# Performance work log

Measured on AMD Instinct MI355X. Metric: run time of the kernel, lower is better.

The kernel has to match this reference:

```python
import jax, jax.numpy as jnp
import numpy as np

NT, NC, NM = 500_000, 100_000, 20_000   # transaction / client / merchant node counts
E = 500_000                              # edges per relation
IN, EMB, HID, OUT = 128, 64, 64, 2


def _lin_init(k, fan_in, fan_out):
    s = 1.0 / np.sqrt(fan_in)
    k1, k2 = jax.random.split(k)
    W = jax.random.uniform(k1, (fan_in, fan_out), jnp.float32, -s, s)
    b = jax.random.uniform(k2, (fan_out,), jnp.float32, -s, s)
    return W, b


def setup_inputs() -> dict:
    key = jax.random.key(0)
    ks = jax.random.split(key, 24)
    it = iter(range(24))
    d = {}
    d["features"] = jax.random.normal(ks[next(it)], (NT, IN), jnp.float32)
    d["emb_client"] = jax.random.normal(ks[next(it)], (NC, EMB), jnp.float32)
    d["emb_merchant"] = jax.random.normal(ks[next(it)], (NM, EMB), jnp.float32)
    for name, n_src, n_dst in [("c2t", NC, NT), ("m2t", NM, NT), ("t2c", NT, NC), ("t2m", NT, NM)]:
        d[f"src_{name}"] = jax.random.randint(ks[next(it)], (E,), 0, n_src)
        d[f"dst_{name}"] = jax.random.randint(ks[next(it)], (E,), 0, n_dst)
    # per-etype input size: in_size if src==transaction else embedding_size
    in0 = {"c2t": EMB, "m2t": EMB, "t2c": IN, "t2m": IN}
    for e in ["c2t", "m2t", "t2c", "t2m"]:
        d[f"W0_{e}"], d[f"b0_{e}"] = _lin_init(ks[next(it)], in0[e], HID)
        d[f"W1_{e}"], d[f"b1_{e}"] = _lin_init(ks[next(it)], HID, HID)
    d["Wf"], d["bf"] = _lin_init(ks[next(it)], HID, OUT)
    return d


def _seg_mean(msg, dst, n):
    # copy_u 'm' + mean reduce; zero in-degree dst nodes get 0 (DGL semantics)
    s = jax.ops.segment_sum(msg, dst, num_segments=n)
    cnt = jax.ops.segment_sum(jnp.ones((msg.shape[0], 1), msg.dtype), dst, num_segments=n)
    return s / jnp.maximum(cnt, 1.0)


def reference(features, emb_client, emb_merchant,
              src_c2t, dst_c2t, src_m2t, dst_m2t,
              src_t2c, dst_t2c, src_t2m, dst_t2m,
              W0_c2t, b0_c2t, W1_c2t, b1_c2t,
              W0_m2t, b0_m2t, W1_m2t, b1_m2t,
              W0_t2c, b0_t2c, W1_t2c, b1_t2c,
              W0_t2m, b0_t2m, W1_t2m, b1_t2m,
              Wf, bf):
    sizes = {"t": NT, "c": NC, "m": NM}
    edges = {"c2t": ("c", "t", src_c2t, dst_c2t),
             "m2t": ("m", "t", src_m2t, dst_m2t),
             "t2c": ("t", "c", src_t2c, dst_t2c),
             "t2m": ("t", "m", src_t2m, dst_t2m)}

    def rgcn_layer(h, W, b):
        acc = {}
        for e, (s, t, src, dst) in edges.items():
            wh = h[s] @ W[e] + b[e]                 # per-relation Linear on src nodes
            m = _seg_mean(wh[src], dst, sizes[t])   # gather + segment-mean
            acc[t] = acc.get(t, 0.0) + m            # cross-relation 'sum'
        return acc

    W0 = {"c2t": W0_c2t, "m2t": W0_m2t, "t2c": W0_t2c, "t2m": W0_t2m}
    b0 = {"c2t": b0_c2t, "m2t": b0_m2t, "t2c": b0_t2c, "t2m": b0_t2m}
    W1 = {"c2t": W1_c2t, "m2t": W1_m2t, "t2c": W1_t2c, "t2m": W1_t2m}
    b1 = {"c2t": b1_c2t, "m2t": b1_m2t, "t2c": b1_t2c, "t2m": b1_t2m}

    h = {"t": features, "c": emb_client, "m": emb_merchant}
    h = rgcn_layer(h, W0, b0)
    h = {k: jax.nn.leaky_relu(v) for k, v in h.items()}  # applied before layer i!=0
    h = rgcn_layer(h, W1, b1)
    return h["t"] @ Wf + bf                          # final Linear on target ntype
```

## Files before the change

kernel.cpp:

```cpp
#include <hip/hip_runtime.h>
#include <stdint.h>

#define NT 500000
#define NC 100000
#define NM 20000
#define NE 500000

__global__ __launch_bounds__(256) void weq_kernel(const float* __restrict__ W1c,
                                                  const float* __restrict__ b1c,
                                                  const float* __restrict__ W1m,
                                                  const float* __restrict__ b1m,
                                                  const float* __restrict__ Wf,
                                                  float* __restrict__ WeqC,
                                                  float* __restrict__ WeqM,
                                                  float* __restrict__ beq) {
    int t = threadIdx.x;
    if (t < 128) {
        int k = t >> 1, o = t & 1;
        float s = 0.0f;
        for (int j = 0; j < 64; j++) s += W1c[k * 64 + j] * Wf[j * 2 + o];
        WeqC[k * 2 + o] = s;
    } else {
        int k = (t - 128) >> 1, o = t & 1;
        float s = 0.0f;
        for (int j = 0; j < 64; j++) s += W1m[k * 64 + j] * Wf[j * 2 + o];
        WeqM[k * 2 + o] = s;
    }
    if (t < 4) {
        const float* b = (t < 2) ? b1c : b1m;
        int o = t & 1;
        float s = 0.0f;
        for (int j = 0; j < 64; j++) s += b[j] * Wf[j * 2 + o];
        beq[t] = s;
    }
}

__global__ __launch_bounds__(256) void hist4(const int* __restrict__ dTC,
                                             const int* __restrict__ dTM,
                                             const int* __restrict__ dCT,
                                             const int* __restrict__ dMT,
                                             int* __restrict__ cC,
                                             int* __restrict__ cM,
                                             int* __restrict__ cTC,
                                             int* __restrict__ cTM) {
    int id = blockIdx.x * 256 + threadIdx.x;
    int r = id / NE;
    int e = id - r * NE;
    if (r == 0)      atomicAdd(&cC[dTC[e]], 1);
    else if (r == 1) atomicAdd(&cM[dTM[e]], 1);
    else if (r == 2) atomicAdd(&cTC[dCT[e]], 1);
    else if (r == 3) atomicAdd(&cTM[dMT[e]], 1);
}

__global__ __launch_bounds__(256) void blocksum4(const int* __restrict__ cC,
                                                 const int* __restrict__ cM,
                                                 const int* __restrict__ cTC,
                                                 const int* __restrict__ cTM,
                                                 int* __restrict__ blkC,
                                                 int* __restrict__ blkM,
                                                 int* __restrict__ blkTC,
                                                 int* __restrict__ blkTM) {
    int b = blockIdx.x;
    const int* counts; int* blk; int n, bb;
    if (b < 98)       { counts = cC;  blk = blkC;  n = NC; bb = b; }
    else if (b < 118) { counts = cM;  blk = blkM;  n = NM; bb = b - 98; }
    else if (b < 607) { counts = cTC; blk = blkTC; n = NT; bb = b - 118; }
    else              { counts = cTM; blk = blkTM; n = NT; bb = b - 607; }
    int tid = threadIdx.x;
    int base = bb * 1024 + tid * 4;
    int s = 0;
#pragma unroll
    for (int j = 0; j < 4; j++) { int i = base + j; if (i < n) s += counts[i]; }
    for (int off = 32; off; off >>= 1) s += __shfl_down(s, off, 64);
    __shared__ int wsum[4];
    if ((tid & 63) == 0) wsum[tid >> 6] = s;
    __syncthreads();
    if (tid == 0) blk[bb] = wsum[0] + wsum[1] + wsum[2] + wsum[3];
}

__global__ __launch_bounds__(256) void scanblk4(int* __restrict__ blkC,
                                                int* __restrict__ blkM,
                                                int* __restrict__ blkTC,
                                                int* __restrict__ blkTM) {
    int* blk; int nb;
    if (blockIdx.x == 0)      { blk = blkC;  nb = 98; }
    else if (blockIdx.x == 1) { blk = blkM;  nb = 20; }
    else if (blockIdx.x == 2) { blk = blkTC; nb = 489; }
    else                      { blk = blkTM; nb = 489; }
    __shared__ int ps[256];
    int tid = threadIdx.x;
    int i0 = 2 * tid, i1 = i0 + 1;
    int a = (i0 < nb) ? blk[i0] : 0;
    int b = (i1 < nb) ? blk[i1] : 0;
    ps[tid] = a + b;
    __syncthreads();
    for (int off = 1; off < 256; off <<= 1) {
        int t = (tid >= off) ? ps[tid - off] : 0;
        __syncthreads();
        ps[tid] += t;
        __syncthreads();
    }
    int excl = ps[tid] - (a + b);
    if (i0 < nb) blk[i0] = excl;
    if (i1 < nb) blk[i1] = excl + a;
}

__global__ __launch_bounds__(256) void scanfinal4(int* __restrict__ rowPtrC,
                                                  int* __restrict__ cursorC,
                                                  const int* __restrict__ blkC,
                                                  int* __restrict__ rowPtrM,
                                                  int* __restrict__ cursorM,
                                                  const int* __restrict__ blkM,
                                                  int* __restrict__ rowPtrTC,
                                                  int* __restrict__ cursorTC,
                                                  const int* __restrict__ blkTC,
                                                  int* __restrict__ rowPtrTM,
                                                  int* __restrict__ cursorTM,
                                                  const int* __restrict__ blkTM) {
    int b = blockIdx.x;
    int* rowPtr; int* cursor; const int* blkOff; int n, bb;
    if (b < 98)       { rowPtr = rowPtrC;  cursor = cursorC;  blkOff = blkC;  n = NC; bb = b; }
    else if (b < 118) { rowPtr = rowPtrM;  cursor = cursorM;  blkOff = blkM;  n = NM; bb = b - 98; }
    else if (b < 607) { rowPtr = rowPtrTC; cursor = cursorTC; blkOff = blkTC; n = NT; bb = b - 118; }
    else              { rowPtr = rowPtrTM; cursor = cursorTM; blkOff = blkTM; n = NT; bb = b - 607; }
    int tid = threadIdx.x, lane = tid & 63, wv = tid >> 6;
    int base = bb * 1024 + tid * 4;
    int c[4];
#pragma unroll
    for (int j = 0; j < 4; j++) { int i = base + j; c[j] = (i < n) ? rowPtr[i] : 0; }
    int t = c[0] + c[1] + c[2] + c[3];
    int incl = t;
    for (int off = 1; off < 64; off <<= 1) {
        int u = __shfl_up(incl, off, 64);
        if (lane >= off) incl += u;
    }
    int lexcl = incl - t;
    __shared__ int wsum[4], woff[4];
    if (lane == 63) wsum[wv] = incl;
    __syncthreads();
    if (tid == 0) { int a = 0; for (int w = 0; w < 4; w++) { woff[w] = a; a += wsum[w]; } }
    __syncthreads();
    int e = blkOff[bb] + woff[wv] + lexcl;
#pragma unroll
    for (int j = 0; j < 4; j++) {
        int i = base + j;
        if (i < n) {
            rowPtr[i] = e;
            cursor[i] = e;
            if (i == n - 1) rowPtr[n] = e + c[j];
        }
        e += c[j];
    }
}

__global__ __launch_bounds__(256) void scatter4(const int* __restrict__ sTC,
                                                const int* __restrict__ dTC,
                                                int* __restrict__ curC,
                                                int* __restrict__ eidxC,
                                                const int* __restrict__ sTM,
                                                const int* __restrict__ dTM,
                                                int* __restrict__ curM,
                                                int* __restrict__ eidxM,
                                                const int* __restrict__ sCT,
                                                const int* __restrict__ dCT,
                                                int* __restrict__ curTC,
                                                int* __restrict__ eidxTC,
                                                const int* __restrict__ sMT,
                                                const int* __restrict__ dMT,
                                                int* __restrict__ curTM,
                                                int* __restrict__ eidxTM) {
    int id = blockIdx.x * 256 + threadIdx.x;
    int r = id / NE;
    int e = id - r * NE;
    if (r == 0)      { int p = atomicAdd(&curC[dTC[e]], 1);  eidxC[p]  = sTC[e]; }
    else if (r == 1) { int p = atomicAdd(&curM[dTM[e]], 1);  eidxM[p]  = sTM[e]; }
    else if (r == 2) { int p = atomicAdd(&curTC[dCT[e]], 1); eidxTC[p] = sCT[e]; }
    else if (r == 3) { int p = atomicAdd(&curTM[dMT[e]], 1); eidxTM[p] = sMT[e]; }
}

__global__ __launch_bounds__(256) void agg_csr(const float* __restrict__ feat,
                                               const int* __restrict__ rowPtr,
                                               const int* __restrict__ eidx,
                                               float* __restrict__ sum,
                                               int base, int nNodes) {
    int gw = (blockIdx.x * 256 + threadIdx.x) >> 6;
    if (gw >= nNodes) return;
    int lane = threadIdx.x & 63;
    int half = lane >> 5;
    int c4 = (lane & 31) * 4;
    int d = base + gw;
    int s0 = rowPtr[d], s1 = rowPtr[d + 1];
    float a0 = 0.f, a1 = 0.f, a2 = 0.f, a3 = 0.f;
    int i = s0;
    for (; i + 1 < s1; i += 2) {
        int s = eidx[i + half];
        const float4 v = *(const float4*)(feat + (size_t)s * 128 + c4);
        a0 += v.x; a1 += v.y; a2 += v.z; a3 += v.w;
    }
    if (i < s1 && half == 0) {
        int s = eidx[i];
        const float4 v = *(const float4*)(feat + (size_t)s * 128 + c4);
        a0 += v.x; a1 += v.y; a2 += v.z; a3 += v.w;
    }
    a0 += __shfl_xor(a0, 32, 64);
    a1 += __shfl_xor(a1, 32, 64);
    a2 += __shfl_xor(a2, 32, 64);
    a3 += __shfl_xor(a3, 32, 64);
    if (half == 0) {
        float4 o; o.x = a0; o.y = a1; o.z = a2; o.w = a3;
        *(float4*)(sum + (size_t)gw * 128 + c4) = o;
    }
}

__global__ __launch_bounds__(256) void h1proj(const float* __restrict__ sum,
                                              const int* __restrict__ rowPtrB,
                                              const float* __restrict__ W0,
                                              const float* __restrict__ b0,
                                              const float* __restrict__ Weq,
                                              float* __restrict__ p, int n) {
    __shared__ float Ws[128 * 64];
    __shared__ float sums[32 * 128];
    int tid = threadIdx.x;
    int base = blockIdx.x * 32;
    {
        const float4* W4 = (const float4*)W0;
        float4* Ws4 = (float4*)Ws;
        for (int i = tid; i < 128 * 64 / 4; i += 256) Ws4[i] = W4[i];
    }
    {
        const float4* S4 = (const float4*)sum;
        float4* s4 = (float4*)sums;
        for (int i = tid; i < 32 * 128 / 4; i += 256) {
            int r = i >> 5;
            int row = base + r;
            float4 v;
            if (row < n) v = S4[(size_t)base * 32 + i];
            else { v.x = v.y = v.z = v.w = 0.0f; }
            s4[i] = v;
        }
    }
    __syncthreads();
    int col = tid & 63, wv = tid >> 6;
    float acc[8];
#pragma unroll
    for (int r = 0; r < 8; r++) acc[r] = 0.0f;
    const float* srow = &sums[wv * 8 * 128];
    for (int k = 0; k < 128; k += 4) {
        float w0_ = Ws[(k + 0) * 64 + col];
        float w1_ = Ws[(k + 1) * 64 + col];
        float w2_ = Ws[(k + 2) * 64 + col];
        float w3_ = Ws[(k + 3) * 64 + col];
#pragma unroll
        for (int r = 0; r < 8; r++) {
            const float4 s = *(const float4*)&srow[r * 128 + k];
            acc[r] += s.x * w0_ + s.y * w1_ + s.z * w2_ + s.w * w3_;
        }
    }
    float b0c = b0[col];
    float wq0 = Weq[col * 2 + 0], wq1 = Weq[col * 2 + 1];
#pragma unroll
    for (int r = 0; r < 8; r++) {
        int row = base + wv * 8 + r;
        int cn = 0;
        if (row < n) cn = rowPtrB[row + 1] - rowPtrB[row];
        float h = 0.0f;
        if (cn > 0) {
            float v = acc[r] / (float)cn + b0c;
            h = v > 0.0f ? v : 0.01f * v;
        }
        float p0 = h * wq0, p1 = h * wq1;
#pragma unroll
        for (int off = 32; off; off >>= 1) {
            p0 += __shfl_down(p0, off, 64);
            p1 += __shfl_down(p1, off, 64);
        }
        if (col == 0 && row < n) {
            p[(size_t)row * 2 + 0] = p0;
            p[(size_t)row * 2 + 1] = p1;
        }
    }
}

__global__ __launch_bounds__(256) void gather_final(const float* __restrict__ pC,
                                                    const int* __restrict__ rowPtrTC,
                                                    const int* __restrict__ eidxTC,
                                                    const float* __restrict__ pM,
                                                    const int* __restrict__ rowPtrTM,
                                                    const int* __restrict__ eidxTM,
                                                    const float* __restrict__ beq,
                                                    const float* __restrict__ bfv,
                                                    float* __restrict__ out) {
    int i = blockIdx.x * 256 + threadIdx.x;
    if (i >= NT) return;
    float r0 = bfv[0], r1 = bfv[1];
    {
        int s0 = rowPtrTC[i], s1 = rowPtrTC[i + 1];
        if (s1 > s0) {
            float a0 = 0.f, a1 = 0.f;
            for (int e = s0; e < s1; e++) {
                int s = eidxTC[e];
                const float2 v = *(const float2*)(pC + (size_t)s * 2);
                a0 += v.x; a1 += v.y;
            }
            float inv = 1.0f / (float)(s1 - s0);
            r0 += a0 * inv + beq[0];
            r1 += a1 * inv + beq[1];
        }
    }
    {
        int s0 = rowPtrTM[i], s1 = rowPtrTM[i + 1];
        if (s1 > s0) {
            float a0 = 0.f, a1 = 0.f;
            for (int e = s0; e < s1; e++) {
                int s = eidxTM[e];
                const float2 v = *(const float2*)(pM + (size_t)s * 2);
                a0 += v.x; a1 += v.y;
            }
            float inv = 1.0f / (float)(s1 - s0);
            r0 += a0 * inv + beq[2];
            r1 += a1 * inv + beq[3];
        }
    }
    float2 o; o.x = r0; o.y = r1;
    *(float2*)(out + (size_t)i * 2) = o;
}

extern "C" void kernel_launch(void* const* d_in, const int* in_sizes, int n_in,
                              void* d_out, int out_size, void* d_ws, size_t ws_size,
                              hipStream_t stream) {
    const float* feat = (const float*)d_in[0];
    const int* src_c2t = (const int*)d_in[3];
    const int* dst_c2t = (const int*)d_in[4];
    const int* src_m2t = (const int*)d_in[5];
    const int* dst_m2t = (const int*)d_in[6];
    const int* src_t2c = (const int*)d_in[7];
    const int* dst_t2c = (const int*)d_in[8];
    const int* src_t2m = (const int*)d_in[9];
    const int* dst_t2m = (const int*)d_in[10];
    const float* W1_c2t = (const float*)d_in[13];
    const float* b1_c2t = (const float*)d_in[14];
    const float* W1_m2t = (const float*)d_in[17];
    const float* b1_m2t = (const float*)d_in[18];
    const float* W0_t2c = (const float*)d_in[19];
    const float* b0_t2c = (const float*)d_in[20];
    const float* W0_t2m = (const float*)d_in[23];
    const float* b0_t2m = (const float*)d_in[24];
    const float* Wf  = (const float*)d_in[27];
    const float* bfv = (const float*)d_in[28];

    char* ws = (char*)d_ws;
    float* SUM      = (float*)(ws + 0);
    int*   rowPtrC  = (int*)(ws + 25600000);
    int*   rowPtrM  = (int*)(ws + 26000016);
    int*   rowPtrTC = (int*)(ws + 26080032);
    int*   rowPtrTM = (int*)(ws + 28080036);
    int*   cursorC  = (int*)(ws + 30080040);
    int*   cursorM  = (int*)(ws + 30480040);
    int*   cursorTC = (int*)(ws + 30560040);
    int*   cursorTM = (int*)(ws + 32560040);
    int*   eidxC    = (int*)(ws + 34560040);
    int*   eidxM    = (int*)(ws + 36560040);
    int*   eidxTC   = (int*)(ws + 38560040);
    int*   eidxTM   = (int*)(ws + 40560040);
    float* pC       = (float*)(ws + 42560040);
    float* pM       = (float*)(ws + 43360040);
    float* WeqC     = (float*)(ws + 43520040);
    float* WeqM     = (float*)(ws + 43520552);
    float* beq      = (float*)(ws + 43521064);
    int*   blkC     = (int*)(ws + 43521080);
    int*   blkM     = (int*)(ws + 43521472);
    int*   blkTC    = (int*)(ws + 43521552);
    int*   blkTM    = (int*)(ws + 43523508);

    hipMemsetAsync(rowPtrC, 0, 4480040, stream);

    weq_kernel<<<1, 256, 0, stream>>>(W1_c2t, b1_c2t, W1_m2t, b1_m2t, Wf, WeqC, WeqM, beq);

    hist4<<<7813, 256, 0, stream>>>(dst_t2c, dst_t2m, dst_c2t, dst_m2t,
                                    rowPtrC, rowPtrM, rowPtrTC, rowPtrTM);
    blocksum4<<<1096, 256, 0, stream>>>(rowPtrC, rowPtrM, rowPtrTC, rowPtrTM,
                                        blkC, blkM, blkTC, blkTM);
    scanblk4<<<4, 256, 0, stream>>>(blkC, blkM, blkTC, blkTM);
    scanfinal4<<<1096, 256, 0, stream>>>(rowPtrC, cursorC, blkC,
                                         rowPtrM, cursorM, blkM,
                                         rowPtrTC, cursorTC, blkTC,
                                         rowPtrTM, cursorTM, blkTM);
    scatter4<<<7813, 256, 0, stream>>>(src_t2c, dst_t2c, cursorC, eidxC,
                                       src_t2m, dst_t2m, cursorM, eidxM,
                                       src_c2t, dst_c2t, cursorTC, eidxTC,
                                       src_m2t, dst_m2t, cursorTM, eidxTM);

    agg_csr<<<12500, 256, 0, stream>>>(feat, rowPtrC, eidxC, SUM, 0, 50000);
    h1proj<<<1563, 256, 0, stream>>>(SUM, rowPtrC, W0_t2c, b0_t2c, WeqC, pC, 50000);
    agg_csr<<<12500, 256, 0, stream>>>(feat, rowPtrC, eidxC, SUM, 50000, 50000);
    h1proj<<<1563, 256, 0, stream>>>(SUM, rowPtrC + 50000, W0_t2c, b0_t2c, WeqC, pC + 100000, 50000);
    agg_csr<<<5000, 256, 0, stream>>>(feat, rowPtrM, eidxM, SUM, 0, 20000);
    h1proj<<<625, 256, 0, stream>>>(SUM, rowPtrM, W0_t2m, b0_t2m, WeqM, pM, 20000);

    gather_final<<<1954, 256, 0, stream>>>(pC, rowPtrTC, eidxTC,
                                           pM, rowPtrTM, eidxTM,
                                           beq, bfv, (float*)d_out);
}
```

Baseline: 825.7 us.

## Replace CSR build with atomicExch linked-list edge chains per destination

Drops the histogram, block-sum, scan and scatter kernels that built a CSR for each relation. A single kernel now pushes every edge onto a per-destination linked list with atomicExch and stores (src, next) records. Aggregation and the final gather walk these chains and count the degree as they go. This saves four launches and their passes over the count arrays, but it makes each edge visit a dependent pointer chase with poor locality, and aggregation now uses float2 per lane with one edge at a time instead of two edges per wave.

```diff
diff --git a/kernel.cpp b/kernel.cpp
--- a/kernel.cpp
+++ b/kernel.cpp
@@ -35,185 +35,64 @@
     }
 }
 
-__global__ __launch_bounds__(256) void hist4(const int* __restrict__ dTC,
-                                             const int* __restrict__ dTM,
-                                             const int* __restrict__ dCT,
-                                             const int* __restrict__ dMT,
-                                             int* __restrict__ cC,
-                                             int* __restrict__ cM,
-                                             int* __restrict__ cTC,
-                                             int* __restrict__ cTM) {
+__global__ __launch_bounds__(256) void chain4(const int* __restrict__ sTC,
+                                              const int* __restrict__ dTC,
+                                              const int* __restrict__ sTM,
+                                              const int* __restrict__ dTM,
+                                              const int* __restrict__ sCT,
+                                              const int* __restrict__ dCT,
+                                              const int* __restrict__ sMT,
+                                              const int* __restrict__ dMT,
+                                              int* __restrict__ headC,
+                                              int* __restrict__ headM,
+                                              int* __restrict__ headTC,
+                                              int* __restrict__ headTM,
+                                              int2* __restrict__ recC,
+                                              int2* __restrict__ recM,
+                                              int2* __restrict__ recTC,
+                                              int2* __restrict__ recTM) {
     int id = blockIdx.x * 256 + threadIdx.x;
     int r = id / NE;
+    if (r > 3) return;
     int e = id - r * NE;
-    if (r == 0)      atomicAdd(&cC[dTC[e]], 1);
-    else if (r == 1) atomicAdd(&cM[dTM[e]], 1);
-    else if (r == 2) atomicAdd(&cTC[dCT[e]], 1);
-    else if (r == 3) atomicAdd(&cTM[dMT[e]], 1);
-}
-
-__global__ __launch_bounds__(256) void blocksum4(const int* __restrict__ cC,
-                                                 const int* __restrict__ cM,
-                                                 const int* __restrict__ cTC,
-                                                 const int* __restrict__ cTM,
-                                                 int* __restrict__ blkC,
-                                                 int* __restrict__ blkM,
-                                                 int* __restrict__ blkTC,
-                                                 int* __restrict__ blkTM) {
-    int b = blockIdx.x;
-    const int* counts; int* blk; int n, bb;
-    if (b < 98)       { counts = cC;  blk = blkC;  n = NC; bb = b; }
-    else if (b < 118) { counts = cM;  blk = blkM;  n = NM; bb = b - 98; }
-    else if (b < 607) { counts = cTC; blk = blkTC; n = NT; bb = b - 118; }
-    else              { counts = cTM; blk = blkTM; n = NT; bb = b - 607; }
-    int tid = threadIdx.x;
-    int base = bb * 1024 + tid * 4;
-    int s = 0;
-#pragma unroll
-    for (int j = 0; j < 4; j++) { int i = base + j; if (i < n) s += counts[i]; }
-    for (int off = 32; off; off >>= 1) s += __shfl_down(s, off, 64);
-    __shared__ int wsum[4];
-    if ((tid & 63) == 0) wsum[tid >> 6] = s;
-    __syncthreads();
-    if (tid == 0) blk[bb] = wsum[0] + wsum[1] + wsum[2] + wsum[3];
-}
-
-__global__ __launch_bounds__(256) void scanblk4(int* __restrict__ blkC,
-                                                int* __restrict__ blkM,
-                                                int* __restrict__ blkTC,
-                                                int* __restrict__ blkTM) {
-    int* blk; int nb;
-    if (blockIdx.x == 0)      { blk = blkC;  nb = 98; }
-    else if (blockIdx.x == 1) { blk = blkM;  nb = 20; }
-    else if (blockIdx.x == 2) { blk = blkTC; nb = 489; }
-    else                      { blk = blkTM; nb = 489; }
-    __shared__ int ps[256];
-    int tid = threadIdx.x;
-    int i0 = 2 * tid, i1 = i0 + 1;
-    int a = (i0 < nb) ? blk[i0] : 0;
-    int b = (i1 < nb) ? blk[i1] : 0;
-    ps[tid] = a + b;
-    __syncthreads();
-    for (int off = 1; off < 256; off <<= 1) {
-        int t = (tid >= off) ? ps[tid - off] : 0;
-        __syncthreads();
-        ps[tid] += t;
-        __syncthreads();
-    }
-    int excl = ps[tid] - (a + b);
-    if (i0 < nb) blk[i0] = excl;
-    if (i1 < nb) blk[i1] = excl + a;
-}
-
-__global__ __launch_bounds__(256) void scanfinal4(int* __restrict__ rowPtrC,
-                                                  int* __restrict__ cursorC,
-                                                  const int* __restrict__ blkC,
-                                                  int* __restrict__ rowPtrM,
-                                                  int* __restrict__ cursorM,
-                                                  const int* __restrict__ blkM,
-                                                  int* __restrict__ rowPtrTC,
-                                                  int* __restrict__ cursorTC,
-                                                  const int* __restrict__ blkTC,
-                                                  int* __restrict__ rowPtrTM,
-                                                  int* __restrict__ cursorTM,
-                                                  const int* __restrict__ blkTM) {
-    int b = blockIdx.x;
-    int* rowPtr; int* cursor; const int* blkOff; int n, bb;
-    if (b < 98)       { rowPtr = rowPtrC;  cursor = cursorC;  blkOff = blkC;  n = NC; bb = b; }
-    else if (b < 118) { rowPtr = rowPtrM;  cursor = cursorM;  blkOff = blkM;  n = NM; bb = b - 98; }
-    else if (b < 607) { rowPtr = rowPtrTC; cursor = cursorTC; blkOff = blkTC; n = NT; bb = b - 118; }
-    else              { rowPtr = rowPtrTM; cursor = cursorTM; blkOff = blkTM; n = NT; bb = b - 607; }
-    int tid = threadIdx.x, lane = tid & 63, wv = tid >> 6;
-    int base = bb * 1024 + tid * 4;
-    int c[4];
-#pragma unroll
-    for (int j = 0; j < 4; j++) { int i = base + j; c[j] = (i < n) ? rowPtr[i] : 0; }
-    int t = c[0] + c[1] + c[2] + c[3];
-    int incl = t;
-    for (int off = 1; off < 64; off <<= 1) {
-        int u = __shfl_up(incl, off, 64);
-        if (lane >= off) incl += u;
-    }
-    int lexcl = incl - t;
-    __shared__ int wsum[4], woff[4];
-    if (lane == 63) wsum[wv] = incl;
-    __syncthreads();
-    if (tid == 0) { int a = 0; for (int w = 0; w < 4; w++) { woff[w] = a; a += wsum[w]; } }
-    __syncthreads();
-    int e = blkOff[bb] + woff[wv] + lexcl;
-#pragma unroll
-    for (int j = 0; j < 4; j++) {
-        int i = base + j;
-        if (i < n) {
-            rowPtr[i] = e;
-            cursor[i] = e;
-            if (i == n - 1) rowPtr[n] = e + c[j];
-        }
-        e += c[j];
-    }
-}
-
-__global__ __launch_bounds__(256) void scatter4(const int* __restrict__ sTC,
-                                                const int* __restrict__ dTC,
-                                                int* __restrict__ curC,
-                                                int* __restrict__ eidxC,
-                                                const int* __restrict__ sTM,
-                                                const int* __restrict__ dTM,
-                                                int* __restrict__ curM,
-                                                int* __restrict__ eidxM,
-                                                const int* __restrict__ sCT,
-                                                const int* __restrict__ dCT,
-                                                int* __restrict__ curTC,
-                                                int* __restrict__ eidxTC,
-                                                const int* __restrict__ sMT,
-                                                const int* __restrict__ dMT,
-                                                int* __restrict__ curTM,
-                                                int* __restrict__ eidxTM) {
-    int id = blockIdx.x * 256 + threadIdx.x;
-    int r = id / NE;
-    int e = id - r * NE;
-    if (r == 0)      { int p = atomicAdd(&curC[dTC[e]], 1);  eidxC[p]  = sTC[e]; }
-    else if (r == 1) { int p = atomicAdd(&curM[dTM[e]], 1);  eidxM[p]  = sTM[e]; }
-    else if (r == 2) { int p = atomicAdd(&curTC[dCT[e]], 1); eidxTC[p] = sCT[e]; }
-    else if (r == 3) { int p = atomicAdd(&curTM[dMT[e]], 1); eidxTM[p] = sMT[e]; }
-}
-
-__global__ __launch_bounds__(256) void agg_csr(const float* __restrict__ feat,
-                                               const int* __restrict__ rowPtr,
-                                               const int* __restrict__ eidx,
-                                               float* __restrict__ sum,
-                                               int base, int nNodes) {
+    const int* src; const int* dst; int* head; int2* rec;
+    if (r == 0)      { src = sTC; dst = dTC; head = headC;  rec = recC; }
+    else if (r == 1) { src = sTM; dst = dTM; head = headM;  rec = recM; }
+    else if (r == 2) { src = sCT; dst = dCT; head = headTC; rec = recTC; }
+    else             { src = sMT; dst = dMT; head = headTM; rec = recTM; }
+    int d = dst[e], s = src[e];
+    int old = atomicExch(&head[d], e);
+    rec[e] = make_int2(s, old);
+}
+
+__global__ __launch_bounds__(256) void agg_chain(const float* __restrict__ feat,
+                                                 const int* __restrict__ head,
+                                                 const int2* __restrict__ rec,
+                                                 float* __restrict__ sum,
+                                                 int* __restrict__ cntArr,
+                                                 int base, int nNodes) {
     int gw = (blockIdx.x * 256 + threadIdx.x) >> 6;
     if (gw >= nNodes) return;
     int lane = threadIdx.x & 63;
-    int half = lane >> 5;
-    int c4 = (lane & 31) * 4;
-    int d = base + gw;
-    int s0 = rowPtr[d], s1 = rowPtr[d + 1];
-    float a0 = 0.f, a1 = 0.f, a2 = 0.f, a3 = 0.f;
-    int i = s0;
-    for (; i + 1 < s1; i += 2) {
-        int s = eidx[i + half];
-        const float4 v = *(const float4*)(feat + (size_t)s * 128 + c4);
-        a0 += v.x; a1 += v.y; a2 += v.z; a3 += v.w;
-    }
-    if (i < s1 && half == 0) {
-        int s = eidx[i];
-        const float4 v = *(const float4*)(feat + (size_t)s * 128 + c4);
-        a0 += v.x; a1 += v.y; a2 += v.z; a3 += v.w;
-    }
-    a0 += __shfl_xor(a0, 32, 64);
-    a1 += __shfl_xor(a1, 32, 64);
-    a2 += __shfl_xor(a2, 32, 64);
-    a3 += __shfl_xor(a3, 32, 64);
-    if (half == 0) {
-        float4 o; o.x = a0; o.y = a1; o.z = a2; o.w = a3;
-        *(float4*)(sum + (size_t)gw * 128 + c4) = o;
-    }
+    int node = base + gw;
+    int e = head[node];
+    float ax = 0.0f, ay = 0.0f;
+    int cnt = 0;
+    const float* fp = feat + lane * 2;
+    while (e >= 0) {
+        int2 rc = rec[e];
+        const float2 v = *(const float2*)(fp + (size_t)rc.x * 128);
+        ax += v.x; ay += v.y;
+        cnt++;
+        e = rc.y;
+    }
+    float2 o; o.x = ax; o.y = ay;
+    *(float2*)(sum + (size_t)gw * 128 + lane * 2) = o;
+    if (lane == 0) cntArr[node] = cnt;
 }
 
 __global__ __launch_bounds__(256) void h1proj(const float* __restrict__ sum,
-                                              const int* __restrict__ rowPtrB,
+                                              const int* __restrict__ cntB,
                                               const float* __restrict__ W0,
                                               const float* __restrict__ b0,
                                               const float* __restrict__ Weq,
@@ -262,7 +141,7 @@
     for (int r = 0; r < 8; r++) {
         int row = base + wv * 8 + r;
         int cn = 0;
-        if (row < n) cn = rowPtrB[row + 1] - rowPtrB[row];
+        if (row < n) cn = cntB[row];
         float h = 0.0f;
         if (cn > 0) {
             float v = acc[r] / (float)cn + b0c;
@@ -282,11 +161,11 @@
 }
 
 __global__ __launch_bounds__(256) void gather_final(const float* __restrict__ pC,
-                                                    const int* __restrict__ rowPtrTC,
-                                                    const int* __restrict__ eidxTC,
+                                                    const int* __restrict__ headTC,
+                                                    const int2* __restrict__ recTC,
                                                     const float* __restrict__ pM,
-                                                    const int* __restrict__ rowPtrTM,
-                                                    const int* __restrict__ eidxTM,
+                                                    const int* __restrict__ headTM,
+                                                    const int2* __restrict__ recTM,
                                                     const float* __restrict__ beq,
                                                     const float* __restrict__ bfv,
                                                     float* __restrict__ out) {
@@ -294,29 +173,35 @@
     if (i >= NT) return;
     float r0 = bfv[0], r1 = bfv[1];
     {
-        int s0 = rowPtrTC[i], s1 = rowPtrTC[i + 1];
-        if (s1 > s0) {
+        int e = headTC[i];
+        if (e >= 0) {
             float a0 = 0.f, a1 = 0.f;
-            for (int e = s0; e < s1; e++) {
-                int s = eidxTC[e];
-                const float2 v = *(const float2*)(pC + (size_t)s * 2);
+            int c = 0;
+            while (e >= 0) {
+                int2 rc = recTC[e];
+                const float2 v = *(const float2*)(pC + (size_t)rc.x * 2);
                 a0 += v.x; a1 += v.y;
+                c++;
+                e = rc.y;
             }
-            float inv = 1.0f / (float)(s1 - s0);
+            float inv = 1.0f / (float)c;
             r0 += a0 * inv + beq[0];
             r1 += a1 * inv + beq[1];
         }
     }
     {
-        int s0 = rowPtrTM[i], s1 = rowPtrTM[i + 1];
-        if (s1 > s0) {
+        int e = headTM[i];
+        if (e >= 0) {
             float a0 = 0.f, a1 = 0.f;
-            for (int e = s0; e < s1; e++) {
-                int s = eidxTM[e];
-                const float2 v = *(const float2*)(pM + (size_t)s * 2);
+            int c = 0;
+            while (e >= 0) {
+                int2 rc = recTM[e];
+                const float2 v = *(const float2*)(pM + (size_t)rc.x * 2);
                 a0 += v.x; a1 += v.y;
+                c++;
+                e = rc.y;
             }
-            float inv = 1.0f / (float)(s1 - s0);
+            float inv = 1.0f / (float)c;
             r0 += a0 * inv + beq[2];
             r1 += a1 * inv + beq[3];
         }
@@ -349,55 +234,40 @@
     const float* bfv = (const float*)d_in[28];
 
     char* ws = (char*)d_ws;
-    float* SUM      = (float*)(ws + 0);
-    int*   rowPtrC  = (int*)(ws + 25600000);
-    int*   rowPtrM  = (int*)(ws + 26000016);
-    int*   rowPtrTC = (int*)(ws + 26080032);
-    int*   rowPtrTM = (int*)(ws + 28080036);
-    int*   cursorC  = (int*)(ws + 30080040);
-    int*   cursorM  = (int*)(ws + 30480040);
-    int*   cursorTC = (int*)(ws + 30560040);
-    int*   cursorTM = (int*)(ws + 32560040);
-    int*   eidxC    = (int*)(ws + 34560040);
-    int*   eidxM    = (int*)(ws + 36560040);
-    int*   eidxTC   = (int*)(ws + 38560040);
-    int*   eidxTM   = (int*)(ws + 40560040);
-    float* pC       = (float*)(ws + 42560040);
-    float* pM       = (float*)(ws + 43360040);
-    float* WeqC     = (float*)(ws + 43520040);
-    float* WeqM     = (float*)(ws + 43520552);
-    float* beq      = (float*)(ws + 43521064);
-    int*   blkC     = (int*)(ws + 43521080);
-    int*   blkM     = (int*)(ws + 43521472);
-    int*   blkTC    = (int*)(ws + 43521552);
-    int*   blkTM    = (int*)(ws + 43523508);
-
-    hipMemsetAsync(rowPtrC, 0, 4480040, stream);
+    float* SUM     = (float*)(ws + 0);
+    int*   headC   = (int*)(ws + 25600000);
+    int*   headM   = (int*)(ws + 26000000);
+    int*   headTC  = (int*)(ws + 26080000);
+    int*   headTM  = (int*)(ws + 28080000);
+    int2*  recC    = (int2*)(ws + 30080000);
+    int2*  recM    = (int2*)(ws + 34080000);
+    int2*  recTC   = (int2*)(ws + 38080000);
+    int2*  recTM   = (int2*)(ws + 42080000);
+    float* pC      = (float*)(ws + 46080000);
+    float* pM      = (float*)(ws + 46880000);
+    int*   cntC    = (int*)(ws + 47040000);
+    int*   cntM    = (int*)(ws + 47440000);
+    float* WeqC    = (float*)(ws + 47520000);
+    float* WeqM    = (float*)(ws + 47520512);
+    float* beq     = (float*)(ws + 47521024);
+
+    hipMemsetAsync(headC, 0xFF, 4480000, stream);
 
     weq_kernel<<<1, 256, 0, stream>>>(W1_c2t, b1_c2t, W1_m2t, b1_m2t, Wf, WeqC, WeqM, beq);
 
-    hist4<<<7813, 256, 0, stream>>>(dst_t2c, dst_t2m, dst_c2t, dst_m2t,
-                                    rowPtrC, rowPtrM, rowPtrTC, rowPtrTM);
-    blocksum4<<<1096, 256, 0, stream>>>(rowPtrC, rowPtrM, rowPtrTC, rowPtrTM,
-                                        blkC, blkM, blkTC, blkTM);
-    scanblk4<<<4, 256, 0, stream>>>(blkC, blkM, blkTC, blkTM);
-    scanfinal4<<<1096, 256, 0, stream>>>(rowPtrC, cursorC, blkC,
-                                         rowPtrM, cursorM, blkM,
-                                         rowPtrTC, cursorTC, blkTC,
-                                         rowPtrTM, cursorTM, blkTM);
-    scatter4<<<7813, 256, 0, stream>>>(src_t2c, dst_t2c, cursorC, eidxC,
-                                       src_t2m, dst_t2m, cursorM, eidxM,
-                                       src_c2t, dst_c2t, cursorTC, eidxTC,
-                                       src_m2t, dst_m2t, cursorTM, eidxTM);
-
-    agg_csr<<<12500, 256, 0, stream>>>(feat, rowPtrC, eidxC, SUM, 0, 50000);
-    h1proj<<<1563, 256, 0, stream>>>(SUM, rowPtrC, W0_t2c, b0_t2c, WeqC, pC, 50000);
-    agg_csr<<<12500, 256, 0, stream>>>(feat, rowPtrC, eidxC, SUM, 50000, 50000);
-    h1proj<<<1563, 256, 0, stream>>>(SUM, rowPtrC + 50000, W0_t2c, b0_t2c, WeqC, pC + 100000, 50000);
-    agg_csr<<<5000, 256, 0, stream>>>(feat, rowPtrM, eidxM, SUM, 0, 20000);
-    h1proj<<<625, 256, 0, stream>>>(SUM, rowPtrM, W0_t2m, b0_t2m, WeqM, pM, 20000);
-
-    gather_final<<<1954, 256, 0, stream>>>(pC, rowPtrTC, eidxTC,
-                                           pM, rowPtrTM, eidxTM,
+    chain4<<<7813, 256, 0, stream>>>(src_t2c, dst_t2c, src_t2m, dst_t2m,
+                                     src_c2t, dst_c2t, src_m2t, dst_m2t,
+                                     headC, headM, headTC, headTM,
+                                     recC, recM, recTC, recTM);
+
+    agg_chain<<<12500, 256, 0, stream>>>(feat, headC, recC, SUM, cntC, 0, 50000);
+    h1proj<<<1563, 256, 0, stream>>>(SUM, cntC, W0_t2c, b0_t2c, WeqC, pC, 50000);
+    agg_chain<<<12500, 256, 0, stream>>>(feat, headC, recC, SUM, cntC, 50000, 50000);
+    h1proj<<<1563, 256, 0, stream>>>(SUM, cntC + 50000, W0_t2c, b0_t2c, WeqC, pC + 100000, 50000);
+    agg_chain<<<5000, 256, 0, stream>>>(feat, headM, recM, SUM, cntM, 0, 20000);
+    h1proj<<<625, 256, 0, stream>>>(SUM, cntM, W0_t2m, b0_t2m, WeqM, pM, 20000);
+
+    gather_final<<<1954, 256, 0, stream>>>(pC, headTC, recTC,
+                                           pM, headTM, recTM,
                                            beq, bfv, (float*)d_out);
 }
```

Result: faster. 739.0 us (-10.5%).
